# Performance work log

Hardware: AMD Instinct MI355X
Metric: run time of the kernel (lower is better)

## Reference

```python
import jax, jax.numpy as jnp
import numpy as np

N, F, E, FE, H, OUT = 20000, 128, 320000, 16, 128, 128
NTYPES = 2  # types = (0, 1)
NPAIRS = NTYPES * NTYPES


def setup_inputs() -> dict:
    key = jax.random.key(0)
    ks = jax.random.split(key, 12)
    edge_in_dim = 2 * F + FE
    node_in_dim = F + H
    s = lambda *shape: 1.0 / np.sqrt(shape[-2])
    return {
        "x": jax.random.normal(ks[0], (N, 1, F), dtype=jnp.float32),
        "edge_index": jax.random.randint(ks[1], (2, E), 0, N, dtype=jnp.int64),
        "edge_attr": jax.random.normal(ks[2], (E, FE), dtype=jnp.float32),
        "node_type": jax.random.randint(ks[3], (N,), 0, NTYPES, dtype=jnp.int64),
        # edge MLP params, stacked over the 4 (t1,t2) type pairs
        "ew1": jax.random.normal(ks[4], (NPAIRS, edge_in_dim, H), dtype=jnp.float32) * (1.0 / np.sqrt(edge_in_dim)),
        "eb1": jnp.zeros((NPAIRS, H), dtype=jnp.float32),
        "ew2": jax.random.normal(ks[5], (NPAIRS, H, H), dtype=jnp.float32) * (1.0 / np.sqrt(H)),
        "eb2": jnp.zeros((NPAIRS, H), dtype=jnp.float32),
        # node MLP params, stacked over the 2 node types
        "nw1": jax.random.normal(ks[6], (NTYPES, node_in_dim, H), dtype=jnp.float32) * (1.0 / np.sqrt(node_in_dim)),
        "nb1": jnp.zeros((NTYPES, H), dtype=jnp.float32),
        "nw2": jax.random.normal(ks[7], (NTYPES, H, OUT), dtype=jnp.float32) * (1.0 / np.sqrt(H)),
        "nb2": jnp.zeros((NTYPES, OUT), dtype=jnp.float32),
    }


def reference(x, edge_index, edge_attr, node_type, ew1, eb1, ew2, eb2, nw1, nb1, nw2, nb2):
    x0 = x[:, 0]  # [N, F]
    row, col = edge_index[0], edge_index[1]

    # ---- edge model: type-pair-dispatched 2-layer ReLU MLP ----
    edge_in = jnp.concatenate([x0[row], x0[col], edge_attr], axis=-1)  # [E, 2F+FE]
    h1 = jax.nn.relu(jnp.einsum("ei,pih->eph", edge_in, ew1) + eb1)    # [E, P, H]
    h2 = jax.nn.relu(jnp.einsum("eph,phk->epk", h1, ew2) + eb2)        # [E, P, H]
    pair_id = node_type[row] * NTYPES + node_type[col]                  # [E]
    pair_oh = jax.nn.one_hot(pair_id, NPAIRS, dtype=h2.dtype)           # [E, P]
    edge_feat = jnp.einsum("epk,ep->ek", h2, pair_oh)                   # [E, H]

    # ---- aggregation: sum over incoming edges per source (row) node ----
    agg = jax.ops.segment_sum(edge_feat, row, num_segments=N)           # [N, H]

    # ---- node model: type-dispatched 2-layer MLP + residual ----
    node_in = jnp.concatenate([x0, agg], axis=-1)                       # [N, F+H]
    n1 = jax.nn.relu(jnp.einsum("ni,tih->nth", node_in, nw1) + nb1)     # [N, T, H]
    n2 = jnp.einsum("nth,thk->ntk", n1, nw2) + nb2                      # [N, T, OUT]
    type_oh = jax.nn.one_hot(node_type, NTYPES, dtype=n2.dtype)         # [N, T]
    out = jnp.einsum("ntk,nt->nk", n2, type_oh)                         # [N, OUT]
    out = out + x0[:, :OUT]  # residual
    return out[:, None, :]  # [N, 1, OUT]
```

## Files before the change

kernel.cpp:

```cpp
#include <hip/hip_runtime.h>

#define N_NODES 20000
#define N_EDGES 320000
#define NBINS   (4*N_NODES)
#define SCAN_NBLK 313

typedef unsigned short u16;
typedef __attribute__((ext_vector_type(8))) short bf16x8;
typedef __attribute__((ext_vector_type(4))) float f32x4;
typedef __attribute__((ext_vector_type(4))) unsigned int u32x4;
typedef __attribute__((ext_vector_type(2))) unsigned int u32x2;

__device__ __forceinline__ float b2f(u16 b){
  unsigned u = ((unsigned)b) << 16; float f; __builtin_memcpy(&f, &u, 4); return f;
}
__device__ __forceinline__ u16 f2b(float f){
  unsigned u; __builtin_memcpy(&u, &f, 4); u += 0x7FFF + ((u >> 16) & 1); return (u16)(u >> 16);
}
__device__ __forceinline__ unsigned cvtpk(float a, float b){
  unsigned r;
  asm("v_cvt_pk_bf16_f32 %0, %1, %2" : "=v"(r) : "v"(a), "v"(b));
  return r;
}

#define NX   (N_NODES*128)
#define NW1T (4*288*128)
#define NW2T (4*128*128)
#define NN1  (2*256*128)
#define NN2  (2*128*128)

__global__ void k_preconv(const float* __restrict__ x,
                          const float* __restrict__ ew1, const float* __restrict__ ew2,
                          const float* __restrict__ nw1, const float* __restrict__ nw2,
                          u16* __restrict__ x0b,
                          u16* __restrict__ wt1t, u16* __restrict__ wt2t,
                          u16* __restrict__ nw1t, u16* __restrict__ nw2t)
{
  int t = blockIdx.x * 256 + threadIdx.x;
  if (t < NX) { x0b[t] = f2b(x[t]); return; }
  t -= NX;
  if (t < NW1T) {
    int p = t / 36864, r = t % 36864; int k = r >> 7, n = r & 127;
    float v = (k < 272) ? ew1[(p * 272 + k) * 128 + n] : 0.f;
    wt1t[(p * 128 + n) * 288 + k] = f2b(v);
    return;
  }
  t -= NW1T;
  if (t < NW2T) {
    int p = t >> 14, r = t & 16383; int k = r >> 7, n = r & 127;
    wt2t[(p * 128 + n) * 128 + k] = f2b(ew2[(p * 128 + k) * 128 + n]);
    return;
  }
  t -= NW2T;
  if (t < NN1) {
    int ty = t >> 15, r = t & 32767; int k = r >> 7, n = r & 127;
    nw1t[(ty * 128 + n) * 256 + k] = f2b(nw1[(ty * 256 + k) * 128 + n]);
    return;
  }
  t -= NN1;
  if (t < NN2) {
    int ty = t >> 14, r = t & 16383; int k = r >> 7, n = r & 127;
    nw2t[(ty * 128 + n) * 128 + k] = f2b(nw2[(ty * 128 + k) * 128 + n]);
  }
}

__global__ void k_hist(const int* __restrict__ ei, const int* __restrict__ ntp,
                       int* __restrict__ hist, int* __restrict__ hist_nt,
                       u16* __restrict__ srank)
{
  int t = blockIdx.x * 256 + threadIdx.x;
  int lane = threadIdx.x & 63;
  if (t < N_EDGES) {
    int r = ei[t], c = ei[N_EDGES + t];
    int tr = ntp[r], tc = ntp[c];
    int key = (tr * 2 + tc) * N_NODES + r;
    int rk = atomicAdd(&hist[key], 1);
    srank[t] = (u16)rk;
  }
  bool valid = t < N_NODES;
  int ty = valid ? ntp[t] : -1;
  unsigned long long m0 = __ballot(ty == 0);
  unsigned long long m1 = __ballot(ty == 1);
  if (lane == 0) {
    int c0 = __popcll(m0), c1 = __popcll(m1);
    if (c0) atomicAdd(&hist_nt[0], c0);
    if (c1) atomicAdd(&hist_nt[1], c1);
  }
}

__global__ void k_scan1(const int* __restrict__ hist, int* __restrict__ parts)
{
  __shared__ int s[256];
  int i = blockIdx.x * 256 + threadIdx.x;
  s[threadIdx.x] = (i < NBINS) ? hist[i] : 0;
  __syncthreads();
  for (int off = 128; off > 0; off >>= 1) {
    if (threadIdx.x < off) s[threadIdx.x] += s[threadIdx.x + off];
    __syncthreads();
  }
  if (threadIdx.x == 0) parts[blockIdx.x] = s[0];
}

__global__ void k_scan2(int* __restrict__ parts)
{
  __shared__ int s[512];
  int t = threadIdx.x;
  int v = (t < SCAN_NBLK) ? parts[t] : 0;
  s[t] = v; __syncthreads();
  for (int off = 1; off < 512; off <<= 1) {
    int xv = (t >= off) ? s[t - off] : 0;
    __syncthreads();
    s[t] += xv;
    __syncthreads();
  }
  if (t < SCAN_NBLK) parts[t] = s[t] - v;
}

__global__ void k_scan3(const int* __restrict__ hist, const int* __restrict__ parts,
                        int* __restrict__ bstart)
{
  __shared__ int s[256];
  int i = blockIdx.x * 256 + threadIdx.x;
  int v = (i < NBINS) ? hist[i] : 0;
  s[threadIdx.x] = v; __syncthreads();
  for (int off = 1; off < 256; off <<= 1) {
    int xv = (threadIdx.x >= off) ? s[threadIdx.x - off] : 0;
    __syncthreads();
    s[threadIdx.x] += xv;
    __syncthreads();
  }
  int excl = s[threadIdx.x] - v + parts[blockIdx.x];
  if (i < NBINS) bstart[i] = excl;
  if (i == 0) bstart[NBINS] = N_EDGES;
}

__global__ void k_place(const int* __restrict__ ei, const int* __restrict__ ntp,
                        const u16* __restrict__ srank, const int* __restrict__ bstart,
                        int2* __restrict__ sedge,
                        int* __restrict__ cur_nt, const int* __restrict__ hist_nt,
                        int* __restrict__ nidx)
{
  int t = blockIdx.x * 256 + threadIdx.x;
  int lane = threadIdx.x & 63;
  if (t < N_EDGES) {
    int r = ei[t], c = ei[N_EDGES + t];
    int tr = ntp[r], tc = ntp[c];
    int key = (tr * 2 + tc) * N_NODES + r;
    int pos = bstart[key] + (int)srank[t];
    int2 v; v.x = r | (c << 15); v.y = t;
    sedge[pos] = v;
  }
  bool valid = t < N_NODES;
  int ty = valid ? ntp[t] : -1;
  unsigned long long m0 = __ballot(ty == 0);
  unsigned long long m1 = __ballot(ty == 1);
  int b0 = 0, b1 = 0;
  if (lane == 0) {
    int c0 = __popcll(m0), c1 = __popcll(m1);
    if (c0) b0 = atomicAdd(&cur_nt[0], c0);
    if (c1) b1 = atomicAdd(&cur_nt[1], c1);
  }
  b0 = __shfl(b0, 0); b1 = __shfl(b1, 0);
  if (valid) {
    unsigned long long lt = (1ull << lane) - 1ull;
    int pos = (ty == 0) ? (b0 + __popcll(m0 & lt))
                        : (hist_nt[0] + b1 + __popcll(m1 & lt));
    nidx[pos] = t;
  }
}

__launch_bounds__(512, 1)
__global__ void k_edge(const u16* __restrict__ x0b, const float* __restrict__ ea,
                       const u16* __restrict__ wt1t, const u16* __restrict__ wt2t,
                       const float* __restrict__ eb1, const float* __restrict__ eb2,
                       const int* __restrict__ bstart, const int2* __restrict__ sedge,
                       u16* __restrict__ h2s)
{
  __shared__ u16 sW1[128 * 296];
  __shared__ u16 sEIN[2 * 128 * 72];
  __shared__ u16 sEA[128 * 40];
  __shared__ float sEb1[128];
  __shared__ float sEb2[128];
  __shared__ int2 sMeta[128];

  const int p    = blockIdx.y;
  const int tid  = threadIdx.x;
  const int lane = tid & 63;
  const int wid  = tid >> 6;
  const int wc   = wid & 1;
  const int we   = wid >> 1;
  const int llo  = lane & 15;
  const int lhi  = lane >> 4;
  const int eidx = tid >> 2;
  const int q    = tid & 3;

  const int base_p = bstart[p * N_NODES];
  const int end_p  = bstart[(p + 1) * N_NODES];

  for (int i = tid; i < 128 * 36; i += 512) {
    int n = i / 36, c = i % 36;
    *(u32x4*)&sW1[n * 296 + c * 8] = *(const u32x4*)&wt1t[(p * 128 + n) * 288 + c * 8];
  }
  if (tid < 128) { sEb1[tid] = eb1[p * 128 + tid]; sEb2[tid] = eb2[p * 128 + tid]; }

  bf16x8 w2[4][4];
  #pragma unroll
  for (int i = 0; i < 4; ++i)
    #pragma unroll
    for (int ck = 0; ck < 4; ++ck)
      w2[i][ck] = *(const bf16x8*)&wt2t[(p * 128 + wc * 64 + i * 16 + llo) * 128 + ck * 32 + lhi * 8];

  u16* sH1 = sEIN;

  for (int ts = base_p + blockIdx.x * 128; ts < end_p; ts += 64 * 128) {
    const int cnt = min(128, end_p - ts);
    if (tid < 128) {
      int2 v = {0, 0};
      if (tid < cnt) v = sedge[ts + tid];
      sMeta[tid] = v;
    }
    __syncthreads();
    const int2 me = sMeta[eidx];
    const int myRow = me.x & 32767, myCol = me.x >> 15, myEid = me.y;

    {
      const u16* src = &x0b[myRow * 128 + q * 16];
      u32x4 l0 = *(const u32x4*)src;
      u32x4 l1 = *(const u32x4*)(src + 8);
      u16* d = &sEIN[eidx * 72 + q * 16];
      *(u32x4*)d = l0; *(u32x4*)(d + 8) = l1;
      u32x4 pk = (u32x4){0u, 0u, 0u, 0u};
      if (q < 2) {
        f32x4 f0 = *(const f32x4*)&ea[myEid * 16 + q * 8];
        f32x4 f1 = *(const f32x4*)&ea[myEid * 16 + q * 8 + 4];
        pk[0] = cvtpk(f0[0], f0[1]); pk[1] = cvtpk(f0[2], f0[3]);
        pk[2] = cvtpk(f1[0], f1[1]); pk[3] = cvtpk(f1[2], f1[3]);
      }
      *(u32x4*)&sEA[eidx * 40 + q * 8] = pk;
    }
    __syncthreads();

    f32x4 acc[4][2];
    #pragma unroll
    for (int i = 0; i < 4; ++i)
      #pragma unroll
      for (int j = 0; j < 2; ++j)
        acc[i][j] = (f32x4){0.f, 0.f, 0.f, 0.f};

    #pragma unroll
    for (int ch = 0; ch < 4; ++ch) {
      const int cur = ch & 1;
      u32x4 n0, n1;
      const int cn = ch + 1;
      if (cn < 4) {
        const int node = (cn < 2) ? myRow : myCol;
        const u16* src = &x0b[node * 128 + (cn & 1) * 64 + q * 16];
        n0 = *(const u32x4*)src; n1 = *(const u32x4*)(src + 8);
      }
      #pragma unroll
      for (int ks = 0; ks < 2; ++ks) {
        const int kk = ks * 32 + lhi * 8;
        bf16x8 a[4], b[2];
        #pragma unroll
        for (int i = 0; i < 4; ++i)
          a[i] = *(const bf16x8*)&sW1[(wc * 64 + i * 16 + llo) * 296 + ch * 64 + kk];
        #pragma unroll
        for (int j = 0; j < 2; ++j)
          b[j] = *(const bf16x8*)&sEIN[cur * (128 * 72) + (we * 32 + j * 16 + llo) * 72 + kk];
        #pragma unroll
        for (int i = 0; i < 4; ++i)
          #pragma unroll
          for (int j = 0; j < 2; ++j)
            acc[i][j] = __builtin_amdgcn_mfma_f32_16x16x32_bf16(a[i], b[j], acc[i][j], 0, 0, 0);
      }
      if (cn < 4) {
        u16* d = &sEIN[(cur ^ 1) * (128 * 72) + eidx * 72 + q * 16];
        *(u32x4*)d = n0; *(u32x4*)(d + 8) = n1;
      }
      __syncthreads();
    }
    {
      const int kk = lhi * 8;
      bf16x8 a[4], b[2];
      #pragma unroll
      for (int i = 0; i < 4; ++i)
        a[i] = *(const bf16x8*)&sW1[(wc * 64 + i * 16 + llo) * 296 + 256 + kk];
      #pragma unroll
      for (int j = 0; j < 2; ++j)
        b[j] = *(const bf16x8*)&sEA[(we * 32 + j * 16 + llo) * 40 + kk];
      #pragma unroll
      for (int i = 0; i < 4; ++i)
        #pragma unroll
        for (int j = 0; j < 2; ++j)
          acc[i][j] = __builtin_amdgcn_mfma_f32_16x16x32_bf16(a[i], b[j], acc[i][j], 0, 0, 0);
    }

    #pragma unroll
    for (int i = 0; i < 4; ++i) {
      const int chb = wc * 64 + i * 16 + lhi * 4;
      const f32x4 bb = *(const f32x4*)&sEb1[chb];
      #pragma unroll
      for (int j = 0; j < 2; ++j) {
        const int edge = we * 32 + j * 16 + llo;
        float v0 = acc[i][j][0] + bb[0]; v0 = v0 > 0.f ? v0 : 0.f;
        float v1 = acc[i][j][1] + bb[1]; v1 = v1 > 0.f ? v1 : 0.f;
        float v2 = acc[i][j][2] + bb[2]; v2 = v2 > 0.f ? v2 : 0.f;
        float v3 = acc[i][j][3] + bb[3]; v3 = v3 > 0.f ? v3 : 0.f;
        u32x2 pk; pk[0] = cvtpk(v0, v1); pk[1] = cvtpk(v2, v3);
        *(u32x2*)&sH1[edge * 136 + chb] = pk;
      }
    }
    __syncthreads();

    bf16x8 bh[2][4];
    #pragma unroll
    for (int j = 0; j < 2; ++j)
      #pragma unroll
      for (int ck = 0; ck < 4; ++ck)
        bh[j][ck] = *(const bf16x8*)&sH1[(we * 32 + j * 16 + llo) * 136 + ck * 32 + lhi * 8];

    #pragma unroll
    for (int i = 0; i < 4; ++i)
      #pragma unroll
      for (int j = 0; j < 2; ++j)
        acc[i][j] = (f32x4){0.f, 0.f, 0.f, 0.f};
    #pragma unroll
    for (int ck = 0; ck < 4; ++ck)
      #pragma unroll
      for (int i = 0; i < 4; ++i)
        #pragma unroll
        for (int j = 0; j < 2; ++j)
          acc[i][j] = __builtin_amdgcn_mfma_f32_16x16x32_bf16(w2[i][ck], bh[j][ck], acc[i][j], 0, 0, 0);

    #pragma unroll
    for (int i = 0; i < 4; ++i) {
      const int chb = wc * 64 + i * 16 + lhi * 4;
      const f32x4 bb = *(const f32x4*)&sEb2[chb];
      #pragma unroll
      for (int j = 0; j < 2; ++j) {
        const int edge = we * 32 + j * 16 + llo;
        float v0 = acc[i][j][0] + bb[0]; v0 = v0 > 0.f ? v0 : 0.f;
        float v1 = acc[i][j][1] + bb[1]; v1 = v1 > 0.f ? v1 : 0.f;
        float v2 = acc[i][j][2] + bb[2]; v2 = v2 > 0.f ? v2 : 0.f;
        float v3 = acc[i][j][3] + bb[3]; v3 = v3 > 0.f ? v3 : 0.f;
        u32x2 pk; pk[0] = cvtpk(v0, v1); pk[1] = cvtpk(v2, v3);
        if (edge < cnt) *(u32x2*)&h2s[(ts + edge) * 128 + chb] = pk;
      }
    }
  }
}

__launch_bounds__(512, 1)
__global__ void k_node(const u16* __restrict__ x0b, const float* __restrict__ xf,
                       const u16* __restrict__ h2s,
                       const u16* __restrict__ nw1t, const u16* __restrict__ nw2t,
                       const float* __restrict__ nb1, const float* __restrict__ nb2,
                       const int* __restrict__ bstart,
                       const int* __restrict__ nidx, const int* __restrict__ hist_nt,
                       float* __restrict__ out)
{
  const int ty    = blockIdx.y;
  const int cnt0  = hist_nt[0];
  const int cnt_t = ty ? (N_NODES - cnt0) : cnt0;
  const int base_t = ty ? cnt0 : 0;

  __shared__ u16 sNIN[64 * 264];
  __shared__ u16 sNW1[128 * 264];
  __shared__ u16 sNW2[128 * 136];
  __shared__ float sNb1[128];
  __shared__ float sNb2[128];
  __shared__ int sNid[64];

  const int tid  = threadIdx.x;
  const int lane = tid & 63;
  const int wid  = tid >> 6;
  const int llo  = lane & 15;
  const int lhi  = lane >> 4;

  for (int i = tid; i < 128 * 256; i += 512) {
    int n = i >> 8, k = i & 255;
    sNW1[n * 264 + k] = nw1t[(ty * 128 + n) * 256 + k];
  }
  for (int i = tid; i < 128 * 128; i += 512) {
    int n = i >> 7, k = i & 127;
    sNW2[n * 136 + k] = nw2t[(ty * 128 + n) * 128 + k];
  }
  if (tid < 128) { sNb1[tid] = nb1[ty * 128 + tid]; sNb2[tid] = nb2[ty * 128 + tid]; }
  __syncthreads();

  for (int t0 = blockIdx.x * 64; t0 < cnt_t; t0 += 128 * 64) {
    const int cnt = min(64, cnt_t - t0);
    if (tid < 64) {
      int nid = 0;
      if (tid < cnt) nid = nidx[base_t + t0 + tid];
      sNid[tid] = nid;
    }
    __syncthreads();

    {
      const int m = tid >> 3, qq = tid & 7;
      const int nid = sNid[m];
      const u16* xs = &x0b[nid * 128 + qq * 16];
      u16* dst = &sNIN[m * 264 + qq * 16];
      #pragma unroll
      for (int j = 0; j < 2; ++j) *(u32x4*)(dst + j * 8) = *(const u32x4*)(xs + j * 8);

      float a[16];
      #pragma unroll
      for (int j = 0; j < 16; ++j) a[j] = 0.f;
      #pragma unroll
      for (int pr = 0; pr < 2; ++pr) {
        const int key = (ty * 2 + pr) * N_NODES + nid;
        const int s = bstart[key], e = bstart[key + 1];
        for (int pos = s; pos < e; ++pos) {
          const u16* hp = &h2s[pos * 128 + qq * 16];
          #pragma unroll
          for (int j = 0; j < 2; ++j) {
            u32x4 v = *(const u32x4*)(hp + j * 8);
            #pragma unroll
            for (int w = 0; w < 4; ++w) {
              unsigned uu = v[w];
              a[j * 8 + w * 2 + 0] += b2f((u16)(uu & 0xFFFFu));
              a[j * 8 + w * 2 + 1] += b2f((u16)(uu >> 16));
            }
          }
        }
      }
      u16* ad = &sNIN[m * 264 + 128 + qq * 16];
      #pragma unroll
      for (int j = 0; j < 8; ++j) {
        unsigned pk = cvtpk(a[2 * j], a[2 * j + 1]);
        *(unsigned*)(ad + 2 * j) = pk;
      }
    }
    __syncthreads();

    f32x4 acc[4];
    #pragma unroll
    for (int i = 0; i < 4; ++i) acc[i] = (f32x4){0.f, 0.f, 0.f, 0.f};

    #pragma unroll
    for (int ck = 0; ck < 8; ++ck) {
      const int kk = ck * 32 + lhi * 8;
      bf16x8 a[4], b;
      #pragma unroll
      for (int i = 0; i < 4; ++i)
        a[i] = *(const bf16x8*)&sNIN[(i * 16 + llo) * 264 + kk];
      b = *(const bf16x8*)&sNW1[(wid * 16 + llo) * 264 + kk];
      #pragma unroll
      for (int i = 0; i < 4; ++i)
        acc[i] = __builtin_amdgcn_mfma_f32_16x16x32_bf16(a[i], b, acc[i], 0, 0, 0);
    }
    __syncthreads();

    u16* sH1 = sNIN;
    #pragma unroll
    for (int i = 0; i < 4; ++i) {
      const int c = wid * 16 + llo;
      const float bias = sNb1[c];
      #pragma unroll
      for (int r = 0; r < 4; ++r) {
        const int m = i * 16 + lhi * 4 + r;
        float v = acc[i][r] + bias;
        v = v > 0.f ? v : 0.f;
        sH1[m * 136 + c] = f2b(v);
      }
    }
    __syncthreads();

    #pragma unroll
    for (int i = 0; i < 4; ++i) acc[i] = (f32x4){0.f, 0.f, 0.f, 0.f};

    #pragma unroll
    for (int ck = 0; ck < 4; ++ck) {
      const int kk = ck * 32 + lhi * 8;
      bf16x8 a[4], b;
      #pragma unroll
      for (int i = 0; i < 4; ++i)
        a[i] = *(const bf16x8*)&sH1[(i * 16 + llo) * 136 + kk];
      b = *(const bf16x8*)&sNW2[(wid * 16 + llo) * 136 + kk];
      #pragma unroll
      for (int i = 0; i < 4; ++i)
        acc[i] = __builtin_amdgcn_mfma_f32_16x16x32_bf16(a[i], b, acc[i], 0, 0, 0);
    }

    #pragma unroll
    for (int i = 0; i < 4; ++i) {
      const int c = wid * 16 + llo;
      const float bias = sNb2[c];
      #pragma unroll
      for (int r = 0; r < 4; ++r) {
        const int m = i * 16 + lhi * 4 + r;
        if (m < cnt) {
          const int nid = sNid[m];
          out[nid * 128 + c] = acc[i][r] + bias + xf[nid * 128 + c];
        }
      }
    }
    __syncthreads();
  }
}

extern "C" void kernel_launch(void* const* d_in, const int* in_sizes, int n_in,
                              void* d_out, int out_size, void* d_ws, size_t ws_size,
                              hipStream_t stream)
{
  const float* x   = (const float*)d_in[0];
  const int*   ei  = (const int*)d_in[1];
  const float* ea  = (const float*)d_in[2];
  const int*   ntp = (const int*)d_in[3];
  const float* ew1 = (const float*)d_in[4];
  const float* eb1 = (const float*)d_in[5];
  const float* ew2 = (const float*)d_in[6];
  const float* eb2 = (const float*)d_in[7];
  const float* nw1 = (const float*)d_in[8];
  const float* nb1 = (const float*)d_in[9];
  const float* nw2 = (const float*)d_in[10];
  const float* nb2 = (const float*)d_in[11];

  char* ws = (char*)d_ws;
  int*  hist    = (int*)(ws + 0);
  int*  hist_nt = (int*)(ws + 320000);
  int*  cur_nt  = (int*)(ws + 320008);
  int*  parts   = (int*)(ws + 320256);
  int*  bstart  = (int*)(ws + 321792);
  u16*  srank   = (u16*)(ws + 641824);
  int2* sedge   = (int2*)(ws + 1281824);
  int*  nidx    = (int*)(ws + 3841824);
  u16*  x0b     = (u16*)(ws + 3921824);
  u16*  wt1t    = (u16*)(ws + 9041824);
  u16*  wt2t    = (u16*)(ws + 9336736);
  u16*  nw1t    = (u16*)(ws + 9467808);
  u16*  nw2t    = (u16*)(ws + 9598880);
  u16*  h2s     = (u16*)(ws + 9664416);

  hipMemsetAsync(ws, 0, 320016, stream);
  k_preconv<<<11216, 256, 0, stream>>>(x, ew1, ew2, nw1, nw2, x0b, wt1t, wt2t, nw1t, nw2t);
  k_hist<<<1250, 256, 0, stream>>>(ei, ntp, hist, hist_nt, srank);
  k_scan1<<<SCAN_NBLK, 256, 0, stream>>>(hist, parts);
  k_scan2<<<1, 512, 0, stream>>>(parts);
  k_scan3<<<SCAN_NBLK, 256, 0, stream>>>(hist, parts, bstart);
  k_place<<<1250, 256, 0, stream>>>(ei, ntp, srank, bstart, sedge, cur_nt, hist_nt, nidx);
  k_edge<<<dim3(64, 4), 512, 0, stream>>>(x0b, ea, wt1t, wt2t, eb1, eb2, bstart, sedge, h2s);
  k_node<<<dim3(128, 2), 512, 0, stream>>>(x0b, x, h2s, nw1t, nw2t, nb1, nb2, bstart, nidx, hist_nt, (float*)d_out);
}
```

Baseline: 188.0 us.

## Restructure edge MLP kernel to per-wave tiles with direct global operand loads

The edge kernel is rewritten so each wave handles 32 edges on its own. Gathered node features are loaded straight from global memory into MFMA operand registers, and the weights are streamed from global/L2 instead of being staged in shared memory. Shared memory is reduced to a small per-wave slab for the layer-1 to layer-2 handoff, which removes most block-wide barriers and lets four 256-thread blocks share a CU. The edge-attribute slice of W1 gets its own padded layout. The cost is repeated weight reads from L2 on every tile and higher register pressure from the 8x2 accumulator tiles.

```diff
diff --git a/kernel.cpp b/kernel.cpp
--- a/kernel.cpp
+++ b/kernel.cpp
@@ -23,26 +23,27 @@
   return r;
 }
 
-#define NX   (N_NODES*128)
-#define NW1T (4*288*128)
-#define NW2T (4*128*128)
-#define NN1  (2*256*128)
-#define NN2  (2*128*128)
+#define NX    (N_NODES*128)
+#define NW1T  (4*256*128)
+#define NW2T  (4*128*128)
+#define NW1CT (4*128*32)
+#define NN1   (2*256*128)
+#define NN2   (2*128*128)
 
 __global__ void k_preconv(const float* __restrict__ x,
                           const float* __restrict__ ew1, const float* __restrict__ ew2,
                           const float* __restrict__ nw1, const float* __restrict__ nw2,
                           u16* __restrict__ x0b,
                           u16* __restrict__ wt1t, u16* __restrict__ wt2t,
+                          u16* __restrict__ wt1ct,
                           u16* __restrict__ nw1t, u16* __restrict__ nw2t)
 {
   int t = blockIdx.x * 256 + threadIdx.x;
   if (t < NX) { x0b[t] = f2b(x[t]); return; }
   t -= NX;
   if (t < NW1T) {
-    int p = t / 36864, r = t % 36864; int k = r >> 7, n = r & 127;
-    float v = (k < 272) ? ew1[(p * 272 + k) * 128 + n] : 0.f;
-    wt1t[(p * 128 + n) * 288 + k] = f2b(v);
+    int p = t >> 15, r = t & 32767; int k = r >> 7, n = r & 127;
+    wt1t[(p * 128 + n) * 256 + k] = f2b(ew1[(p * 272 + k) * 128 + n]);
     return;
   }
   t -= NW1T;
@@ -52,6 +53,13 @@
     return;
   }
   t -= NW2T;
+  if (t < NW1CT) {
+    int p = t >> 12, r = t & 4095; int n = r >> 5, kk = r & 31;
+    float v = (kk < 16) ? ew1[(p * 272 + 256 + kk) * 128 + n] : 0.f;
+    wt1ct[(p * 128 + n) * 32 + kk] = f2b(v);
+    return;
+  }
+  t -= NW1CT;
   if (t < NN1) {
     int ty = t >> 15, r = t & 32767; int k = r >> 7, n = r & 127;
     nw1t[(ty * 128 + n) * 256 + k] = f2b(nw1[(ty * 256 + k) * 128 + n]);
@@ -169,182 +177,155 @@
   }
 }
 
-__launch_bounds__(512, 1)
+__launch_bounds__(256, 4)
 __global__ void k_edge(const u16* __restrict__ x0b, const float* __restrict__ ea,
-                       const u16* __restrict__ wt1t, const u16* __restrict__ wt2t,
+                       const u16* __restrict__ wt1t, const u16* __restrict__ wt1ct,
+                       const u16* __restrict__ wt2t,
                        const float* __restrict__ eb1, const float* __restrict__ eb2,
                        const int* __restrict__ bstart, const int2* __restrict__ sedge,
                        u16* __restrict__ h2s)
 {
-  __shared__ u16 sW1[128 * 296];
-  __shared__ u16 sEIN[2 * 128 * 72];
-  __shared__ u16 sEA[128 * 40];
+  __shared__ u16 slab[4][2][16][136];
   __shared__ float sEb1[128];
   __shared__ float sEb2[128];
-  __shared__ int2 sMeta[128];
 
   const int p    = blockIdx.y;
   const int tid  = threadIdx.x;
   const int lane = tid & 63;
-  const int wid  = tid >> 6;
-  const int wc   = wid & 1;
-  const int we   = wid >> 1;
+  const int wv   = tid >> 6;
   const int llo  = lane & 15;
   const int lhi  = lane >> 4;
-  const int eidx = tid >> 2;
-  const int q    = tid & 3;
+
+  if (tid < 128) sEb1[tid] = eb1[p * 128 + tid];
+  else sEb2[tid - 128] = eb2[p * 128 + tid - 128];
+  __syncthreads();
 
   const int base_p = bstart[p * N_NODES];
   const int end_p  = bstart[(p + 1) * N_NODES];
 
-  for (int i = tid; i < 128 * 36; i += 512) {
-    int n = i / 36, c = i % 36;
-    *(u32x4*)&sW1[n * 296 + c * 8] = *(const u32x4*)&wt1t[(p * 128 + n) * 288 + c * 8];
-  }
-  if (tid < 128) { sEb1[tid] = eb1[p * 128 + tid]; sEb2[tid] = eb2[p * 128 + tid]; }
-
-  bf16x8 w2[4][4];
+  bf16x8 w1c[8];
   #pragma unroll
-  for (int i = 0; i < 4; ++i)
-    #pragma unroll
-    for (int ck = 0; ck < 4; ++ck)
-      w2[i][ck] = *(const bf16x8*)&wt2t[(p * 128 + wc * 64 + i * 16 + llo) * 128 + ck * 32 + lhi * 8];
-
-  u16* sH1 = sEIN;
-
-  for (int ts = base_p + blockIdx.x * 128; ts < end_p; ts += 64 * 128) {
-    const int cnt = min(128, end_p - ts);
-    if (tid < 128) {
-      int2 v = {0, 0};
-      if (tid < cnt) v = sedge[ts + tid];
-      sMeta[tid] = v;
-    }
-    __syncthreads();
-    const int2 me = sMeta[eidx];
-    const int myRow = me.x & 32767, myCol = me.x >> 15, myEid = me.y;
-
-    {
-      const u16* src = &x0b[myRow * 128 + q * 16];
-      u32x4 l0 = *(const u32x4*)src;
-      u32x4 l1 = *(const u32x4*)(src + 8);
-      u16* d = &sEIN[eidx * 72 + q * 16];
-      *(u32x4*)d = l0; *(u32x4*)(d + 8) = l1;
+  for (int i = 0; i < 8; ++i)
+    w1c[i] = *(const bf16x8*)&wt1ct[(p * 128 + i * 16 + llo) * 32 + lhi * 8];
+
+  for (int ts = base_p + blockIdx.x * 128; ts < end_p; ts += gridDim.x * 128) {
+    const int e0 = ts + wv * 32;
+    int pos[2], row[2], col[2], eid[2];
+    #pragma unroll
+    for (int j = 0; j < 2; ++j) {
+      pos[j] = e0 + j * 16 + llo;
+      int pc = pos[j] < end_p ? pos[j] : end_p - 1;
+      int2 m = sedge[pc];
+      row[j] = m.x & 32767; col[j] = m.x >> 15; eid[j] = m.y;
+    }
+
+    bf16x8 xr[2][4], xc[2][4], eaf[2];
+    #pragma unroll
+    for (int j = 0; j < 2; ++j) {
+      #pragma unroll
+      for (int ck = 0; ck < 4; ++ck) {
+        xr[j][ck] = *(const bf16x8*)&x0b[row[j] * 128 + ck * 32 + lhi * 8];
+        xc[j][ck] = *(const bf16x8*)&x0b[col[j] * 128 + ck * 32 + lhi * 8];
+      }
       u32x4 pk = (u32x4){0u, 0u, 0u, 0u};
-      if (q < 2) {
-        f32x4 f0 = *(const f32x4*)&ea[myEid * 16 + q * 8];
-        f32x4 f1 = *(const f32x4*)&ea[myEid * 16 + q * 8 + 4];
+      if (lhi < 2) {
+        f32x4 f0 = *(const f32x4*)&ea[eid[j] * 16 + lhi * 8];
+        f32x4 f1 = *(const f32x4*)&ea[eid[j] * 16 + lhi * 8 + 4];
         pk[0] = cvtpk(f0[0], f0[1]); pk[1] = cvtpk(f0[2], f0[3]);
         pk[2] = cvtpk(f1[0], f1[1]); pk[3] = cvtpk(f1[2], f1[3]);
       }
-      *(u32x4*)&sEA[eidx * 40 + q * 8] = pk;
-    }
-    __syncthreads();
-
-    f32x4 acc[4][2];
-    #pragma unroll
-    for (int i = 0; i < 4; ++i)
+      __builtin_memcpy(&eaf[j], &pk, 16);
+    }
+
+    f32x4 eacc[8][2];
+    #pragma unroll
+    for (int i = 0; i < 8; ++i)
+      #pragma unroll
+      for (int j = 0; j < 2; ++j)
+        eacc[i][j] = (f32x4){0.f, 0.f, 0.f, 0.f};
+
+    #pragma unroll
+    for (int ck = 0; ck < 4; ++ck) {
+      bf16x8 wa[8];
+      #pragma unroll
+      for (int i = 0; i < 8; ++i)
+        wa[i] = *(const bf16x8*)&wt1t[(p * 128 + i * 16 + llo) * 256 + ck * 32 + lhi * 8];
+      #pragma unroll
+      for (int i = 0; i < 8; ++i)
+        #pragma unroll
+        for (int j = 0; j < 2; ++j)
+          eacc[i][j] = __builtin_amdgcn_mfma_f32_16x16x32_bf16(wa[i], xr[j][ck], eacc[i][j], 0, 0, 0);
+    }
+    #pragma unroll
+    for (int ck = 0; ck < 4; ++ck) {
+      bf16x8 wb[8];
+      #pragma unroll
+      for (int i = 0; i < 8; ++i)
+        wb[i] = *(const bf16x8*)&wt1t[(p * 128 + i * 16 + llo) * 256 + 128 + ck * 32 + lhi * 8];
+      #pragma unroll
+      for (int i = 0; i < 8; ++i)
+        #pragma unroll
+        for (int j = 0; j < 2; ++j)
+          eacc[i][j] = __builtin_amdgcn_mfma_f32_16x16x32_bf16(wb[i], xc[j][ck], eacc[i][j], 0, 0, 0);
+    }
+    #pragma unroll
+    for (int i = 0; i < 8; ++i)
+      #pragma unroll
+      for (int j = 0; j < 2; ++j)
+        eacc[i][j] = __builtin_amdgcn_mfma_f32_16x16x32_bf16(w1c[i], eaf[j], eacc[i][j], 0, 0, 0);
+
+    #pragma unroll
+    for (int i = 0; i < 8; ++i) {
+      const f32x4 bb = *(const f32x4*)&sEb1[i * 16 + lhi * 4];
+      #pragma unroll
+      for (int j = 0; j < 2; ++j) {
+        float v0 = eacc[i][j][0] + bb[0]; v0 = v0 > 0.f ? v0 : 0.f;
+        float v1 = eacc[i][j][1] + bb[1]; v1 = v1 > 0.f ? v1 : 0.f;
+        float v2 = eacc[i][j][2] + bb[2]; v2 = v2 > 0.f ? v2 : 0.f;
+        float v3 = eacc[i][j][3] + bb[3]; v3 = v3 > 0.f ? v3 : 0.f;
+        u32x2 pk; pk[0] = cvtpk(v0, v1); pk[1] = cvtpk(v2, v3);
+        *(u32x2*)&slab[wv][j][llo][i * 16 + lhi * 4] = pk;
+      }
+    }
+
+    bf16x8 h1f[2][4];
+    #pragma unroll
+    for (int j = 0; j < 2; ++j)
+      #pragma unroll
+      for (int ck = 0; ck < 4; ++ck)
+        h1f[j][ck] = *(const bf16x8*)&slab[wv][j][llo][ck * 32 + lhi * 8];
+
+    f32x4 acc[8][2];
+    #pragma unroll
+    for (int i = 0; i < 8; ++i)
       #pragma unroll
       for (int j = 0; j < 2; ++j)
         acc[i][j] = (f32x4){0.f, 0.f, 0.f, 0.f};
 
     #pragma unroll
-    for (int ch = 0; ch < 4; ++ch) {
-      const int cur = ch & 1;
-      u32x4 n0, n1;
-      const int cn = ch + 1;
-      if (cn < 4) {
-        const int node = (cn < 2) ? myRow : myCol;
-        const u16* src = &x0b[node * 128 + (cn & 1) * 64 + q * 16];
-        n0 = *(const u32x4*)src; n1 = *(const u32x4*)(src + 8);
-      }
-      #pragma unroll
-      for (int ks = 0; ks < 2; ++ks) {
-        const int kk = ks * 32 + lhi * 8;
-        bf16x8 a[4], b[2];
-        #pragma unroll
-        for (int i = 0; i < 4; ++i)
-          a[i] = *(const bf16x8*)&sW1[(wc * 64 + i * 16 + llo) * 296 + ch * 64 + kk];
+    for (int ck = 0; ck < 4; ++ck) {
+      bf16x8 w2[8];
+      #pragma unroll
+      for (int i = 0; i < 8; ++i)
+        w2[i] = *(const bf16x8*)&wt2t[(p * 128 + i * 16 + llo) * 128 + ck * 32 + lhi * 8];
+      #pragma unroll
+      for (int i = 0; i < 8; ++i)
         #pragma unroll
         for (int j = 0; j < 2; ++j)
-          b[j] = *(const bf16x8*)&sEIN[cur * (128 * 72) + (we * 32 + j * 16 + llo) * 72 + kk];
-        #pragma unroll
-        for (int i = 0; i < 4; ++i)
-          #pragma unroll
-          for (int j = 0; j < 2; ++j)
-            acc[i][j] = __builtin_amdgcn_mfma_f32_16x16x32_bf16(a[i], b[j], acc[i][j], 0, 0, 0);
-      }
-      if (cn < 4) {
-        u16* d = &sEIN[(cur ^ 1) * (128 * 72) + eidx * 72 + q * 16];
-        *(u32x4*)d = n0; *(u32x4*)(d + 8) = n1;
-      }
-      __syncthreads();
-    }
-    {
-      const int kk = lhi * 8;
-      bf16x8 a[4], b[2];
-      #pragma unroll
-      for (int i = 0; i < 4; ++i)
-        a[i] = *(const bf16x8*)&sW1[(wc * 64 + i * 16 + llo) * 296 + 256 + kk];
-      #pragma unroll
-      for (int j = 0; j < 2; ++j)
-        b[j] = *(const bf16x8*)&sEA[(we * 32 + j * 16 + llo) * 40 + kk];
-      #pragma unroll
-      for (int i = 0; i < 4; ++i)
-        #pragma unroll
-        for (int j = 0; j < 2; ++j)
-          acc[i][j] = __builtin_amdgcn_mfma_f32_16x16x32_bf16(a[i], b[j], acc[i][j], 0, 0, 0);
-    }
-
-    #pragma unroll
-    for (int i = 0; i < 4; ++i) {
-      const int chb = wc * 64 + i * 16 + lhi * 4;
-      const f32x4 bb = *(const f32x4*)&sEb1[chb];
+          acc[i][j] = __builtin_amdgcn_mfma_f32_16x16x32_bf16(w2[i], h1f[j][ck], acc[i][j], 0, 0, 0);
+    }
+
+    #pragma unroll
+    for (int i = 0; i < 8; ++i) {
+      const f32x4 bb = *(const f32x4*)&sEb2[i * 16 + lhi * 4];
       #pragma unroll
       for (int j = 0; j < 2; ++j) {
-        const int edge = we * 32 + j * 16 + llo;
         float v0 = acc[i][j][0] + bb[0]; v0 = v0 > 0.f ? v0 : 0.f;
         float v1 = acc[i][j][1] + bb[1]; v1 = v1 > 0.f ? v1 : 0.f;
         float v2 = acc[i][j][2] + bb[2]; v2 = v2 > 0.f ? v2 : 0.f;
         float v3 = acc[i][j][3] + bb[3]; v3 = v3 > 0.f ? v3 : 0.f;
         u32x2 pk; pk[0] = cvtpk(v0, v1); pk[1] = cvtpk(v2, v3);
-        *(u32x2*)&sH1[edge * 136 + chb] = pk;
-      }
-    }
-    __syncthreads();
-
-    bf16x8 bh[2][4];
-    #pragma unroll
-    for (int j = 0; j < 2; ++j)
-      #pragma unroll
-      for (int ck = 0; ck < 4; ++ck)
-        bh[j][ck] = *(const bf16x8*)&sH1[(we * 32 + j * 16 + llo) * 136 + ck * 32 + lhi * 8];
-
-    #pragma unroll
-    for (int i = 0; i < 4; ++i)
-      #pragma unroll
-      for (int j = 0; j < 2; ++j)
-        acc[i][j] = (f32x4){0.f, 0.f, 0.f, 0.f};
-    #pragma unroll
-    for (int ck = 0; ck < 4; ++ck)
-      #pragma unroll
-      for (int i = 0; i < 4; ++i)
-        #pragma unroll
-        for (int j = 0; j < 2; ++j)
-          acc[i][j] = __builtin_amdgcn_mfma_f32_16x16x32_bf16(w2[i][ck], bh[j][ck], acc[i][j], 0, 0, 0);
-
-    #pragma unroll
-    for (int i = 0; i < 4; ++i) {
-      const int chb = wc * 64 + i * 16 + lhi * 4;
-      const f32x4 bb = *(const f32x4*)&sEb2[chb];
-      #pragma unroll
-      for (int j = 0; j < 2; ++j) {
-        const int edge = we * 32 + j * 16 + llo;
-        float v0 = acc[i][j][0] + bb[0]; v0 = v0 > 0.f ? v0 : 0.f;
-        float v1 = acc[i][j][1] + bb[1]; v1 = v1 > 0.f ? v1 : 0.f;
-        float v2 = acc[i][j][2] + bb[2]; v2 = v2 > 0.f ? v2 : 0.f;
-        float v3 = acc[i][j][3] + bb[3]; v3 = v3 > 0.f ? v3 : 0.f;
-        u32x2 pk; pk[0] = cvtpk(v0, v1); pk[1] = cvtpk(v2, v3);
-        if (edge < cnt) *(u32x2*)&h2s[(ts + edge) * 128 + chb] = pk;
+        if (pos[j] < end_p) *(u32x2*)&h2s[pos[j] * 128 + i * 16 + lhi * 4] = pk;
       }
     }
   }
@@ -529,18 +510,19 @@
   int*  nidx    = (int*)(ws + 3841824);
   u16*  x0b     = (u16*)(ws + 3921824);
   u16*  wt1t    = (u16*)(ws + 9041824);
-  u16*  wt2t    = (u16*)(ws + 9336736);
+  u16*  wt2t    = (u16*)(ws + 9303968);
+  u16*  wt1ct   = (u16*)(ws + 9435040);
   u16*  nw1t    = (u16*)(ws + 9467808);
   u16*  nw2t    = (u16*)(ws + 9598880);
   u16*  h2s     = (u16*)(ws + 9664416);
 
   hipMemsetAsync(ws, 0, 320016, stream);
-  k_preconv<<<11216, 256, 0, stream>>>(x, ew1, ew2, nw1, nw2, x0b, wt1t, wt2t, nw1t, nw2t);
+  k_preconv<<<11216, 256, 0, stream>>>(x, ew1, ew2, nw1, nw2, x0b, wt1t, wt2t, wt1ct, nw1t, nw2t);
   k_hist<<<1250, 256, 0, stream>>>(ei, ntp, hist, hist_nt, srank);
   k_scan1<<<SCAN_NBLK, 256, 0, stream>>>(hist, parts);
   k_scan2<<<1, 512, 0, stream>>>(parts);
   k_scan3<<<SCAN_NBLK, 256, 0, stream>>>(hist, parts, bstart);
   k_place<<<1250, 256, 0, stream>>>(ei, ntp, srank, bstart, sedge, cur_nt, hist_nt, nidx);
-  k_edge<<<dim3(64, 4), 512, 0, stream>>>(x0b, ea, wt1t, wt2t, eb1, eb2, bstart, sedge, h2s);
+  k_edge<<<dim3(256, 4), 256, 0, stream>>>(x0b, ea, wt1t, wt1ct, wt2t, eb1, eb2, bstart, sedge, h2s);
   k_node<<<dim3(128, 2), 512, 0, stream>>>(x0b, x, h2s, nw1t, nw2t, nb1, nb2, bstart, nidx, hist_nt, (float*)d_out);
 }
```

New measurement: 463.0 us. 146% more time.
